# Kernel tuning notes

Hardware: AMD Instinct MI355X
Metric: run time of the kernel (lower is better)

The kernel has to match this reference:

```python
import jax, jax.numpy as jnp
import numpy as np

N_OBJ, N_REL = 5000, 20000
HID, POOL, N_RELCLS, N_OBJCLS = 512, 4096, 51, 151


def setup_inputs() -> dict:
    key = jax.random.key(0)
    ks = jax.random.split(key, 8)
    s = lambda fi, fo: (2.0 / (fi + fo)) ** 0.5  # xavier-ish scale
    return {
        'edge_ctx': jax.random.normal(ks[0], (N_OBJ, HID), jnp.float32),
        'union_features': jax.random.normal(ks[1], (N_REL, POOL), jnp.float32),
        'W_pe': jax.random.normal(ks[2], (2 * HID, HID), jnp.float32) * (10.0 * (1.0 / HID) ** 0.5),
        'b_pe': jnp.zeros((2 * HID,), jnp.float32),
        'W_pc': jax.random.normal(ks[3], (POOL, 2 * HID), jnp.float32) * s(2 * HID, POOL),
        'b_pc': jnp.zeros((POOL,), jnp.float32),
        'W_cc': jax.random.normal(ks[4], (N_RELCLS, POOL), jnp.float32) * s(POOL, N_RELCLS),
        'b_cc': jnp.zeros((N_RELCLS,), jnp.float32),
        'freq_emb': jax.random.normal(ks[5], (N_OBJCLS * N_OBJCLS, N_RELCLS), jnp.float32) * 0.1,
        'obj_preds': jax.random.randint(ks[6], (N_OBJ,), 0, N_OBJCLS, jnp.int64 if jax.config.jax_enable_x64 else jnp.int32),
        'pair_idx': jax.random.randint(ks[7], (N_REL, 2), 0, N_OBJ, jnp.int64 if jax.config.jax_enable_x64 else jnp.int32),
    }


def reference(edge_ctx, union_features, W_pe, b_pe, W_pc, b_pc, W_cc, b_cc,
              freq_emb, obj_preds, pair_idx):
    # post_emb -> relu -> split into head/tail halves ([N,2,HID] view)
    edge_rep = jax.nn.relu(edge_ctx @ W_pe.T + b_pe)          # [N, 2*HID]
    head_rep, tail_rep = edge_rep[:, :HID], edge_rep[:, HID:]

    hi, ti = pair_idx[:, 0], pair_idx[:, 1]
    prod = jnp.concatenate([head_rep[hi], tail_rep[ti]], axis=-1)  # [R, 2*HID]
    prod_rep = prod @ W_pc.T + b_pc                               # [R, POOL]

    ctx_dists = (prod_rep * union_features) @ W_cc.T + b_cc      # [R, 51]

    # frequency bias: embedding lookup at head_cls * num_obj_cls + tail_cls
    pair_lbl = obj_preds[hi] * N_OBJCLS + obj_preds[ti]
    frq_dists = freq_emb[pair_lbl]                               # [R, 51]
    # dropout p=0.3 is identity in eval mode
    return ctx_dists + frq_dists
```

## Files before the change

### kernel.cpp

```cpp
#include <hip/hip_runtime.h>

typedef unsigned short u16;
typedef unsigned int u32;
typedef __attribute__((ext_vector_type(4))) float f32x4;
typedef __attribute__((ext_vector_type(8))) __bf16 bf16x8;
typedef __attribute__((ext_vector_type(8))) u16 u16x8;

__device__ __forceinline__ u16 f2bf(float x) {
  u32 u = __float_as_uint(x);
  u32 r = (u + 0x7FFFu + ((u >> 16) & 1u)) >> 16;
  return (u16)r;
}

__device__ __forceinline__ float bf2f(u16 b) {
  return __uint_as_float((u32)b << 16);
}

__device__ __forceinline__ void gl16(const void* g, void* l) {
  auto* gp = (__attribute__((address_space(1))) u32*)(g);
  auto* lp = (__attribute__((address_space(3))) u32*)(l);
  __builtin_amdgcn_global_load_lds(gp, lp, 16, 0, 0);
}

__device__ __forceinline__ f32x4 mfma16(bf16x8 a, bf16x8 b, f32x4 c) {
  return __builtin_amdgcn_mfma_f32_16x16x32_bf16(a, b, c, 0, 0, 0);
}

__device__ __forceinline__ u16x8 cvt8(const float* p) {
  float4 a = *(const float4*)p, b = *(const float4*)(p + 4);
  u16x8 v;
  v[0] = f2bf(a.x); v[1] = f2bf(a.y); v[2] = f2bf(a.z); v[3] = f2bf(a.w);
  v[4] = f2bf(b.x); v[5] = f2bf(b.y); v[6] = f2bf(b.z); v[7] = f2bf(b.w);
  return v;
}

__global__ void k_prep(const float* __restrict__ ec, const float* __restrict__ wpe,
                       const float* __restrict__ wpc, const float* __restrict__ wcc,
                       u16* __restrict__ ecb, u16* __restrict__ wpeb,
                       u16* __restrict__ wpcb, u16* __restrict__ wccb) {
  int i = blockIdx.x * 256 + threadIdx.x;
  if (i < 320000) {
    *(u16x8*)(ecb + (long)i * 8) = cvt8(ec + (long)i * 8);
  } else if (i < 385536) {
    int j = i - 320000;
    *(u16x8*)(wpeb + (long)j * 8) = cvt8(wpe + (long)j * 8);
  } else if (i < 909824) {
    int j = i - 385536;
    *(u16x8*)(wpcb + (long)j * 8) = cvt8(wpc + (long)j * 8);
  } else if (i < 942592) {
    int j = i - 909824;
    long base = (long)j * 8;
    int row = (int)(base >> 12);
    int col = (int)(base & 4095);
    u16x8 v;
    if (row < 51) {
      v = cvt8(wcc + (long)row * 4096 + col);
    } else {
#pragma unroll
      for (int k = 0; k < 8; ++k) v[k] = 0;
    }
    *(u16x8*)(wccb + base) = v;
  }
}

__device__ __forceinline__ void cstep(const char* sA, const char* sB,
                                      const int (&aOff)[4], const int (&bOff)[4],
                                      f32x4 (&acc)[4][4]) {
  bf16x8 af[4], bv[4];
#pragma unroll
  for (int mi = 0; mi < 4; ++mi) af[mi] = *(const bf16x8*)(sA + aOff[mi]);
#pragma unroll
  for (int ni = 0; ni < 4; ++ni) bv[ni] = *(const bf16x8*)(sB + bOff[ni]);
  __builtin_amdgcn_s_setprio(1);
#pragma unroll
  for (int mi = 0; mi < 4; ++mi)
#pragma unroll
    for (int ni = 0; ni < 4; ++ni)
      acc[mi][ni] = mfma16(af[mi], bv[ni], acc[mi][ni]);
  __builtin_amdgcn_s_setprio(0);
}

__device__ __forceinline__ void cstep64(const char* buf,
                                        const int (&aOff)[4][2], const int (&bOff)[4][2],
                                        f32x4 (&acc)[4][4]) {
  bf16x8 af[4][2], bv[4][2];
#pragma unroll
  for (int mi = 0; mi < 4; ++mi)
#pragma unroll
    for (int ks = 0; ks < 2; ++ks) af[mi][ks] = *(const bf16x8*)(buf + aOff[mi][ks]);
#pragma unroll
  for (int ni = 0; ni < 4; ++ni)
#pragma unroll
    for (int ks = 0; ks < 2; ++ks) bv[ni][ks] = *(const bf16x8*)(buf + bOff[ni][ks]);
  __builtin_amdgcn_s_setprio(1);
#pragma unroll
  for (int ks = 0; ks < 2; ++ks)
#pragma unroll
    for (int mi = 0; mi < 4; ++mi)
#pragma unroll
      for (int ni = 0; ni < 4; ++ni)
        acc[mi][ni] = mfma16(af[mi][ks], bv[ni][ks], acc[mi][ni]);
  __builtin_amdgcn_s_setprio(0);
}

__global__ __launch_bounds__(256, 2) void k_gemm1(const u16* __restrict__ A, const u16* __restrict__ B,
                                                  const float* __restrict__ bias, u16* __restrict__ outp) {
  __shared__ char lds[65536];
  int bx = blockIdx.x;
  int rb = bx >> 3, nb = bx & 7;
  int rowBase = rb * 128, nBase = nb * 128;
  int t = threadIdx.x, lane = t & 63, wid = t >> 6;
  int wr = wid >> 1, wc = wid & 1, lm = lane & 15, lg = lane >> 4;
  int ar0 = t >> 2, ar1 = 64 + ar0, c4 = t & 3;
  int sw0 = (c4 * 16) ^ (((ar0 >> 1) & 3) << 4);
  int sw1 = (c4 * 16) ^ (((ar1 >> 1) & 3) << 4);
  const char* aS0 = (const char*)(A + (long)min(rowBase + ar0, 4999) * 512) + sw0;
  const char* aS1 = (const char*)(A + (long)min(rowBase + ar1, 4999) * 512) + sw1;
  const char* bS0 = (const char*)(B + (long)(nBase + ar0) * 512) + sw0;
  const char* bS1 = (const char*)(B + (long)(nBase + ar1) * 512) + sw1;
  int t16 = t * 16;
  int aOff[4], bOff[4];
#pragma unroll
  for (int mi = 0; mi < 4; ++mi) { int r = wr * 64 + mi * 16 + lm; aOff[mi] = r * 64 + ((lg * 16) ^ (((r >> 1) & 3) << 4)); }
#pragma unroll
  for (int ni = 0; ni < 4; ++ni) { int r = wc * 64 + ni * 16 + lm; bOff[ni] = r * 64 + ((lg * 16) ^ (((r >> 1) & 3) << 4)); }
  f32x4 acc[4][4] = {};

#define STAGE_G(k, sb) do { \
    gl16(aS0 + (k) * 2, (sb) + t16); gl16(aS1 + (k) * 2, (sb) + 4096 + t16); \
    gl16(bS0 + (k) * 2, (sb) + 8192 + t16); gl16(bS1 + (k) * 2, (sb) + 12288 + t16); \
  } while (0)

  STAGE_G(0, lds);
  STAGE_G(32, lds + 16384);
  STAGE_G(64, lds + 32768);

  int cur = 0, stg = 3;
  for (int kt = 0; kt < 16; ++kt) {
    if (kt < 13) {
      char* sb = lds + stg * 16384;
      STAGE_G((kt + 3) * 32, sb);
    }
    if (kt < 13)       asm volatile("s_waitcnt vmcnt(12)" ::: "memory");
    else if (kt == 13) asm volatile("s_waitcnt vmcnt(8)" ::: "memory");
    else if (kt == 14) asm volatile("s_waitcnt vmcnt(4)" ::: "memory");
    else               asm volatile("s_waitcnt vmcnt(0)" ::: "memory");
    __builtin_amdgcn_s_barrier();
    char* cb = lds + cur * 16384;
    cstep(cb, cb + 8192, aOff, bOff, acc);
    __builtin_amdgcn_s_barrier();
    cur = (cur == 3) ? 0 : cur + 1;
    stg = (stg == 3) ? 0 : stg + 1;
  }
#undef STAGE_G

#pragma unroll
  for (int mi = 0; mi < 4; ++mi)
#pragma unroll
    for (int ni = 0; ni < 4; ++ni) {
      int n = nBase + wc * 64 + ni * 16 + lm;
      float bvv = bias[n];
#pragma unroll
      for (int rg = 0; rg < 4; ++rg) {
        int r = rowBase + wr * 64 + mi * 16 + lg * 4 + rg;
        if (r < 5000) {
          float v = acc[mi][ni][rg] + bvv;
          v = v > 0.f ? v : 0.f;
          outp[(long)r * 1024 + n] = f2bf(v);
        }
      }
    }
}

__global__ __launch_bounds__(256, 2) void k_gemm2(const u16* __restrict__ erep, const u16* __restrict__ wpc,
                                                  const float* __restrict__ bpc, u16* __restrict__ Hout,
                                                  u16* __restrict__ Tout) {
  __shared__ char lds[65536];
  int bx = blockIdx.x;
  int h = (bx >= 1280) ? 1 : 0;
  int rr = bx - h * 1280;
  int rb = rr >> 5, nb = rr & 31;
  int rowBase = rb * 128, nBase = nb * 128;
  u16* outp = h ? Tout : Hout;
  int t = threadIdx.x, lane = t & 63, wid = t >> 6;
  int wr = wid >> 1, wc = wid & 1, lm = lane & 15, lg = lane >> 4;
  int ar = t >> 3, c8 = t & 7;
  int srcswz = ((c8 ^ (ar & 7)) << 4);
  const char* aP[4];
  const char* bP[4];
#pragma unroll
  for (int i = 0; i < 4; ++i) {
    int Ra = min(rowBase + i * 32 + ar, 4999);
    aP[i] = (const char*)(erep + (long)Ra * 1024 + h * 512) + srcswz;
    int Rb = nBase + i * 32 + ar;
    bP[i] = (const char*)(wpc + (long)Rb * 1024 + h * 512) + srcswz;
  }
  int t16 = t * 16;
  int aOff[4][2], bOff[4][2];
#pragma unroll
  for (int mi = 0; mi < 4; ++mi)
#pragma unroll
    for (int ks = 0; ks < 2; ++ks) {
      int r = wr * 64 + mi * 16 + lm;
      aOff[mi][ks] = r * 128 + (((ks * 4 + lg) ^ (r & 7)) << 4);
    }
#pragma unroll
  for (int ni = 0; ni < 4; ++ni)
#pragma unroll
    for (int ks = 0; ks < 2; ++ks) {
      int r = wc * 64 + ni * 16 + lm;
      bOff[ni][ks] = 16384 + r * 128 + (((ks * 4 + lg) ^ (r & 7)) << 4);
    }
  f32x4 acc[4][4] = {};

#define STAGE2(kk, buf) do { \
    _Pragma("unroll") \
    for (int i = 0; i < 4; ++i) { \
      gl16(aP[i] + (kk) * 2, (buf) + i * 4096 + t16); \
      gl16(bP[i] + (kk) * 2, (buf) + 16384 + i * 4096 + t16); \
    } \
  } while (0)

  STAGE2(0, lds);
  for (int kt = 0; kt < 8; ++kt) {
    if (kt < 7) STAGE2((kt + 1) * 64, lds + (((kt + 1) & 1) ? 32768 : 0));
    if (kt < 7) asm volatile("s_waitcnt vmcnt(8)" ::: "memory");
    else        asm volatile("s_waitcnt vmcnt(0)" ::: "memory");
    __builtin_amdgcn_s_barrier();
    cstep64(lds + ((kt & 1) ? 32768 : 0), aOff, bOff, acc);
    __builtin_amdgcn_s_barrier();
  }
#undef STAGE2

#pragma unroll
  for (int mi = 0; mi < 4; ++mi)
#pragma unroll
    for (int ni = 0; ni < 4; ++ni) {
      int n = nBase + wc * 64 + ni * 16 + lm;
      float bvv = h ? 0.f : bpc[n];
#pragma unroll
      for (int rg = 0; rg < 4; ++rg) {
        int r = rowBase + wr * 64 + mi * 16 + lg * 4 + rg;
        if (r < 5000) {
          float v = acc[mi][ni][rg] + bvv;
          outp[(long)r * 4096 + n] = f2bf(v);
        }
      }
    }
}

__global__ __launch_bounds__(256) void k_final(
    const u16* __restrict__ H, const u16* __restrict__ T,
    const u16* __restrict__ wcc,
    const float* __restrict__ un,
    const int* __restrict__ pidx,
    float* __restrict__ partial) {
  __shared__ char sU[16384];
  int bx = blockIdx.x;
  int rb = bx >> 3, ps = bx & 7;
  int rowBase = rb * 64;
  int t = threadIdx.x, lane = t & 63, wid = t >> 6;
  int lm = lane & 15, lg = lane >> 4;
  int r16 = t >> 4, c16 = t & 15;

  u32 hoff[4], toff[4], uoff[4];
#pragma unroll
  for (int p = 0; p < 4; ++p) {
    int rG = min(rowBase + p * 16 + r16, 19999);
    hoff[p] = (u32)pidx[2 * rG] * 8192u + (u32)c16 * 16u;
    toff[p] = (u32)pidx[2 * rG + 1] * 8192u + (u32)c16 * 16u;
    uoff[p] = (u32)rG * 16384u + (u32)c16 * 32u;
  }
  const char* Hc = (const char*)H;
  const char* Tc = (const char*)T;
  const char* Uc = (const char*)un;
  int pc0 = ps * 512;

  f32x4 outAcc[4] = {};

  for (int chk = 0; chk < 4; ++chk) {
    int pcBase = pc0 + chk * 128;
    if (chk) __syncthreads();
#pragma unroll
    for (int p = 0; p < 4; ++p) {
      int r = p * 16 + r16;
      u16x8 h8 = *(const u16x8*)(Hc + hoff[p] + (u32)pcBase * 2u);
      u16x8 t8 = *(const u16x8*)(Tc + toff[p] + (u32)pcBase * 2u);
      float4 u0 = *(const float4*)(Uc + uoff[p] + (u32)pcBase * 4u);
      float4 u1 = *(const float4*)(Uc + uoff[p] + (u32)pcBase * 4u + 16u);
      float uu[8];
      *(float4*)(uu) = u0;
      *(float4*)(uu + 4) = u1;
      u16x8 pv;
#pragma unroll
      for (int j = 0; j < 8; ++j)
        pv[j] = f2bf((bf2f(h8[j]) + bf2f(t8[j])) * uu[j]);
      *(u16x8*)(sU + r * 256 + ((c16 * 16) ^ ((r & 7) << 4))) = pv;
    }
    __syncthreads();

#pragma unroll
    for (int kb = 0; kb < 4; ++kb) {
      int r = wid * 16 + lm;
      bf16x8 aU = *(const bf16x8*)(sU + r * 256 + ((kb * 64 + lg * 16) ^ ((r & 7) << 4)));
      bf16x8 bW[4];
#pragma unroll
      for (int ni = 0; ni < 4; ++ni)
        bW[ni] = *(const bf16x8*)(wcc + (long)(ni * 16 + lm) * 4096 + pcBase + kb * 32 + lg * 8);
      __builtin_amdgcn_s_setprio(1);
#pragma unroll
      for (int ni = 0; ni < 4; ++ni)
        outAcc[ni] = mfma16(aU, bW[ni], outAcc[ni]);
      __builtin_amdgcn_s_setprio(0);
    }
  }

#pragma unroll
  for (int rg = 0; rg < 4; ++rg) {
    int r = wid * 16 + lg * 4 + rg;
    int rG = rowBase + r;
    if (rG < 20000) {
      long base = ((long)ps * 20000 + rG) * 64;
#pragma unroll
      for (int ni = 0; ni < 4; ++ni) {
        int c = ni * 16 + lm;
        if (c < 51) partial[base + c] = outAcc[ni][rg];
      }
    }
  }
}

__global__ void k_red(const float* __restrict__ partial, const float* __restrict__ bcc,
                      const float* __restrict__ freq, const int* __restrict__ preds,
                      const int* __restrict__ pidx, float* __restrict__ outp) {
  int idx = blockIdx.x * 256 + threadIdx.x;
  if (idx >= 20000 * 64) return;
  int row = idx >> 6, c = idx & 63;
  if (c >= 51) return;
  float s = 0.f;
#pragma unroll
  for (int i = 0; i < 8; ++i) s += partial[((long)i * 20000 + row) * 64 + c];
  int lbl = preds[pidx[2 * row]] * 151 + preds[pidx[2 * row + 1]];
  outp[(long)row * 51 + c] = s + bcc[c] + freq[(long)lbl * 51 + c];
}

extern "C" void kernel_launch(void* const* d_in, const int* in_sizes, int n_in,
                              void* d_out, int out_size, void* d_ws, size_t ws_size,
                              hipStream_t stream) {
  const float* edge_ctx = (const float*)d_in[0];
  const float* unionf   = (const float*)d_in[1];
  const float* W_pe     = (const float*)d_in[2];
  const float* b_pe     = (const float*)d_in[3];
  const float* W_pc     = (const float*)d_in[4];
  const float* b_pc     = (const float*)d_in[5];
  const float* W_cc     = (const float*)d_in[6];
  const float* b_cc     = (const float*)d_in[7];
  const float* freq     = (const float*)d_in[8];
  const int*   preds    = (const int*)d_in[9];
  const int*   pidx     = (const int*)d_in[10];
  float* out = (float*)d_out;
  char* ws = (char*)d_ws;

  u16* Hb    = (u16*)(ws + 0);
  u16* Tb    = (u16*)(ws + 40960000);
  u16* erep  = (u16*)(ws + 81920000);
  u16* wpcb  = (u16*)(ws + 92160000);
  u16* wccb  = (u16*)(ws + 100548608);
  u16* ecb   = (u16*)(ws + 101072896);
  u16* wpeb  = (u16*)(ws + 106192896);
  float* par = (float*)(ws + 107241472);

  k_prep<<<3682, 256, 0, stream>>>(edge_ctx, W_pe, W_pc, W_cc, ecb, wpeb, wpcb, wccb);
  k_gemm1<<<320, 256, 0, stream>>>(ecb, wpeb, b_pe, erep);
  k_gemm2<<<2560, 256, 0, stream>>>(erep, wpcb, b_pc, Hb, Tb);
  k_final<<<2504, 256, 0, stream>>>(Hb, Tb, wccb, unionf, pidx, par);
  k_red<<<5000, 256, 0, stream>>>(par, b_cc, freq, preds, pidx, out);
}
```

Before: 263.9 us.

## Double-buffer LDS and prefetch next chunk's gathers in final kernel

Gives the k_final kernel two LDS buffers and issues the global gathers for the next 128-column chunk before the MFMA phase of the current chunk. The aim is to hide gather and load latency behind compute and to drop one barrier per iteration. In exchange it doubles LDS use to 32KB per block and adds registers for the prefetched values, which may lower occupancy. The vmcnt(0) wait at the top of each iteration also waits on the bW global loads.

```diff
diff --git a/kernel.cpp b/kernel.cpp
--- a/kernel.cpp
+++ b/kernel.cpp
@@ -255,7 +255,7 @@
     const float* __restrict__ un,
     const int* __restrict__ pidx,
     float* __restrict__ partial) {
-  __shared__ char sU[16384];
+  __shared__ char sU[2][16384];
   int bx = blockIdx.x;
   int rb = bx >> 3, ps = bx & 7;
   int rowBase = rb * 64;
@@ -276,33 +276,47 @@
   const char* Uc = (const char*)un;
   int pc0 = ps * 512;
 
+  u16x8 h8[4], t8[4];
+  float4 u0[4], u1[4];
+
+#define ISSUE(pcB) do { \
+    _Pragma("unroll") \
+    for (int p = 0; p < 4; ++p) { \
+      h8[p] = *(const u16x8*)(Hc + hoff[p] + (u32)(pcB) * 2u); \
+      t8[p] = *(const u16x8*)(Tc + toff[p] + (u32)(pcB) * 2u); \
+      u0[p] = *(const float4*)(Uc + uoff[p] + (u32)(pcB) * 4u); \
+      u1[p] = *(const float4*)(Uc + uoff[p] + (u32)(pcB) * 4u + 16u); \
+    } \
+  } while (0)
+
   f32x4 outAcc[4] = {};
+
+  ISSUE(pc0);
 
   for (int chk = 0; chk < 4; ++chk) {
     int pcBase = pc0 + chk * 128;
-    if (chk) __syncthreads();
+    asm volatile("s_waitcnt vmcnt(0)" ::: "memory");
+    char* sUb = sU[chk & 1];
 #pragma unroll
     for (int p = 0; p < 4; ++p) {
       int r = p * 16 + r16;
-      u16x8 h8 = *(const u16x8*)(Hc + hoff[p] + (u32)pcBase * 2u);
-      u16x8 t8 = *(const u16x8*)(Tc + toff[p] + (u32)pcBase * 2u);
-      float4 u0 = *(const float4*)(Uc + uoff[p] + (u32)pcBase * 4u);
-      float4 u1 = *(const float4*)(Uc + uoff[p] + (u32)pcBase * 4u + 16u);
       float uu[8];
-      *(float4*)(uu) = u0;
-      *(float4*)(uu + 4) = u1;
+      *(float4*)(uu) = u0[p];
+      *(float4*)(uu + 4) = u1[p];
       u16x8 pv;
 #pragma unroll
       for (int j = 0; j < 8; ++j)
-        pv[j] = f2bf((bf2f(h8[j]) + bf2f(t8[j])) * uu[j]);
-      *(u16x8*)(sU + r * 256 + ((c16 * 16) ^ ((r & 7) << 4))) = pv;
-    }
-    __syncthreads();
+        pv[j] = f2bf((bf2f(h8[p][j]) + bf2f(t8[p][j])) * uu[j]);
+      *(u16x8*)(sUb + r * 256 + ((c16 * 16) ^ ((r & 7) << 4))) = pv;
+    }
+    if (chk < 3) ISSUE(pcBase + 128);
+    asm volatile("s_waitcnt lgkmcnt(0)" ::: "memory");
+    __builtin_amdgcn_s_barrier();
 
 #pragma unroll
     for (int kb = 0; kb < 4; ++kb) {
       int r = wid * 16 + lm;
-      bf16x8 aU = *(const bf16x8*)(sU + r * 256 + ((kb * 64 + lg * 16) ^ ((r & 7) << 4)));
+      bf16x8 aU = *(const bf16x8*)(sUb + r * 256 + ((kb * 64 + lg * 16) ^ ((r & 7) << 4)));
       bf16x8 bW[4];
 #pragma unroll
       for (int ni = 0; ni < 4; ++ni)
@@ -314,6 +328,7 @@
       __builtin_amdgcn_s_setprio(0);
     }
   }
+#undef ISSUE
 
 #pragma unroll
   for (int rg = 0; rg < 4; ++rg) {
```

Measured after the change: 259.3 us (median of 2 runs). About the same (-1.8%).
